# Kernel optimization log

Measured on AMD Instinct MI355X. Metric: run time of the kernel, lower is better.

The kernel has to match this reference:

```python
import jax, jax.numpy as jnp
import numpy as np

B, K, S, E = 16, 16, 512, 512   # batch, k_history, max_spikes_in_batch, embed_dim
L, H, KVH, D = 16, 8, 2, 64     # num_latents, heads, kv heads, head_dim
BIN = 50                        # bin_size (RoPE table length)


def setup_inputs() -> dict:
    key = jax.random.key(0)
    ks = jax.random.split(key, 8)
    spike = jax.random.normal(ks[0], (B, K, S, E), dtype=jnp.float32)
    offsets = jax.random.randint(ks[1], (B, K, S), 0, BIN)
    spike_lengths = jax.random.randint(ks[2], (B, K), 1, S + 1)  # >=1 so no fully-masked row
    # standard RoPE tables of shape (BIN, D)
    inv_freq = 1.0 / (10000.0 ** (np.arange(0, D, 2, dtype=np.float32) / D))
    freqs = np.outer(np.arange(BIN, dtype=np.float32), inv_freq)      # (BIN, D/2)
    emb = np.concatenate([freqs, freqs], axis=-1)                     # (BIN, D)
    cos = jnp.asarray(np.cos(emb), dtype=jnp.float32)
    sin = jnp.asarray(np.sin(emb), dtype=jnp.float32)
    latent_query = jax.random.normal(ks[3], (L, E), dtype=jnp.float32)
    Wq = jax.random.normal(ks[4], (H * D, E), dtype=jnp.float32) * (E ** -0.5)
    Wk = jax.random.normal(ks[5], (KVH * D, E), dtype=jnp.float32) * (E ** -0.5)
    Wv = jax.random.normal(ks[6], (KVH * D, E), dtype=jnp.float32) * (E ** -0.5)
    Wo = jax.random.normal(ks[7], (E, H * D), dtype=jnp.float32) * ((H * D) ** -0.5)
    return dict(spike=spike, offsets=offsets, spike_lengths=spike_lengths,
                cos=cos, sin=sin, latent_query=latent_query,
                Wq=Wq, Wk=Wk, Wv=Wv, Wo=Wo)


def rotate_half(x):
    h = x.shape[-1] // 2
    return jnp.concatenate([-x[..., h:], x[..., :h]], axis=-1)


def reference(spike, offsets, spike_lengths, cos, sin, latent_query, Wq, Wk, Wv, Wo):
    n_rep = H // KVH
    # fixed learnable queries, shared across batch / k_history
    xq = (latent_query @ Wq.T).reshape(L, H, D)                         # (L,H,D)
    xk = jnp.einsum('bkse,he->bksh', spike, Wk).reshape(B, K, S, KVH, D)
    xv = jnp.einsum('bkse,he->bksh', spike, Wv).reshape(B, K, S, KVH, D)
    # inline RoPE on keys only (is_decoder=False), driven by per-token offsets
    cos_sel = cos[offsets][..., None, :]                                # (B,K,S,1,D)
    sin_sel = sin[offsets][..., None, :]
    xk = xk * cos_sel + rotate_half(xk) * sin_sel
    # repeat_kv: interleaved head repetition (matches torch expand+reshape)
    xk = jnp.repeat(xk, n_rep, axis=3)                                  # (B,K,S,H,D)
    xv = jnp.repeat(xv, n_rep, axis=3)
    scores = jnp.einsum('lhd,bkshd->bkhls', xq, xk) / jnp.sqrt(jnp.float32(D))
    # ragged-length mask: positions >= spike_lengths are invalid
    pos = jnp.arange(S)
    mask = pos[None, None, None, None, :] >= spike_lengths[:, :, None, None, None]
    scores = jnp.where(mask, -jnp.inf, scores)
    attn = jax.nn.softmax(scores, axis=-1)                              # (B,K,H,L,S)
    out = jnp.einsum('bkhls,bkshd->bklhd', attn, xv).reshape(B, K, L, H * D)
    return out @ Wo.T                                                   # (B,K,L,E)
```

## Files before the change

### kernel.cpp

```cpp
#include <hip/hip_runtime.h>
#include <hip/hip_bf16.h>
#include <stdint.h>

typedef __attribute__((ext_vector_type(8))) short bf16x8;
typedef __attribute__((ext_vector_type(4))) float f32x4;

union FragU { uint4 u; bf16x8 v; };

#define Bn 16
#define Kn 16
#define Sn 512
#define En 512
#define Ln 16
#define Hn 8
#define Dn 64
#define BKTOT 256
#define MTOT (BKTOT*Sn)

__device__ __forceinline__ uint32_t pack_bf16(float lo, float hi) {
  uint32_t a = __float_as_uint(lo) + 0x8000u;
  uint32_t b = __float_as_uint(hi) + 0x8000u;
  return __builtin_amdgcn_perm(b, a, 0x07060302u);
}
__device__ __forceinline__ uint16_t bf16_1(float x) {
  __hip_bfloat16 h = __float2bfloat16(x);
  return *(uint16_t*)&h;
}
__device__ __forceinline__ void gload_lds16(const void* g, void* l) {
  __builtin_amdgcn_global_load_lds(
      (const __attribute__((address_space(1))) uint32_t*)g,
      (__attribute__((address_space(3))) uint32_t*)l, 16, 0, 0);
}

__global__ __launch_bounds__(256)
void xq_kernel(const float* __restrict__ latent, const float* __restrict__ Wq,
               float* __restrict__ xq)
{
  const int j = blockIdx.x;
  const int t = threadIdx.x;
  const float w0 = Wq[j*En + t];
  const float w1 = Wq[j*En + t + 256];
  float part[Ln];
#pragma unroll
  for (int l = 0; l < Ln; ++l)
    part[l] = w0 * latent[l*En + t] + w1 * latent[l*En + t + 256];
#pragma unroll
  for (int l = 0; l < Ln; ++l) {
    float v = part[l];
#pragma unroll
    for (int off = 32; off > 0; off >>= 1) v += __shfl_down(v, off, 64);
    part[l] = v;
  }
  __shared__ float red[4][Ln];
  const int lane = t & 63, wv = t >> 6;
  if (lane == 0) {
#pragma unroll
    for (int l = 0; l < Ln; ++l) red[wv][l] = part[l];
  }
  __syncthreads();
  if (t < Ln)
    xq[t*En + j] = red[0][t] + red[1][t] + red[2][t] + red[3][t];
}

__global__ __launch_bounds__(256)
void wconv_kernel(const float* __restrict__ Wk, const float* __restrict__ Wv,
                  const float* __restrict__ Wo,
                  uint4* __restrict__ Wsw, uint4* __restrict__ Wob)
{
  const int t = threadIdx.x;
  const int b = blockIdx.x;
  if (b < 64) {
    const int idx = b*256 + t;
    const int kb = idx >> 11;
    const int rem = idx & 2047;
    const int n = rem >> 3, p = rem & 7;
    const int c = p ^ (n & 7);
    const float* src = (n < 128 ? Wk + (size_t)n*En : Wv + (size_t)(n-128)*En) + kb*64 + c*8;
    float4 v0 = *(const float4*)src;
    float4 v1 = *(const float4*)(src+4);
    uint4 o;
    o.x = pack_bf16(v0.x,v0.y); o.y = pack_bf16(v0.z,v0.w);
    o.z = pack_bf16(v1.x,v1.y); o.w = pack_bf16(v1.z,v1.w);
    Wsw[idx] = o;
  } else {
    const int idx = (b-64)*256 + t;
    const float* src = Wo + (size_t)idx*8;
    float4 v0 = *(const float4*)src;
    float4 v1 = *(const float4*)(src+4);
    uint4 o;
    o.x = pack_bf16(v0.x,v0.y); o.y = pack_bf16(v0.z,v0.w);
    o.z = pack_bf16(v1.x,v1.y); o.w = pack_bf16(v1.z,v1.w);
    Wob[idx] = o;
  }
}

__global__ __launch_bounds__(256)
void kvproj_kernel(const float* __restrict__ spike, const int* __restrict__ offsets,
                   const float* __restrict__ cosT, const float* __restrict__ sinT,
                   const uint4* __restrict__ Wsw, const int* __restrict__ lengths,
                   uint16_t* __restrict__ Kbuf, uint16_t* __restrict__ Vt)
{
  __shared__ __align__(16) uint16_t Bs[256*64];
  __shared__ __align__(16) uint16_t As[64*72];
  const int t = threadIdx.x;
  const int bk   = blockIdx.x >> 3;
  const int tile = blockIdx.x & 7;
  if (tile * 64 >= lengths[bk]) return;
  const int m0 = blockIdx.x * 64;
  const int lane = t & 63, wv = t >> 6;
  const int quad = lane >> 4, lr = lane & 15;

  f32x4 acc[4][4];
#pragma unroll
  for (int i=0;i<4;i++)
#pragma unroll
    for (int j=0;j<4;j++) acc[i][j] = (f32x4){0.f,0.f,0.f,0.f};

  const int arow = t >> 3;
  const int aseg = t & 7;

  for (int kb = 0; kb < 8; ++kb) {
    const char* gb = (const char*)(Wsw + kb*2048) + (wv*64 + lane)*16;
    char* lb = (char*)Bs + wv*1024;
#pragma unroll
    for (int i = 0; i < 8; ++i)
      gload_lds16(gb + i*4096, lb + i*4096);
#pragma unroll
    for (int j = 0; j < 2; ++j) {
      const int row = arow + 32*j;
      const float* src = &spike[(size_t)(m0+row)*En + kb*64 + aseg*8];
      float4 v0 = *(const float4*)src;
      float4 v1 = *(const float4*)(src+4);
      uint4 o;
      o.x = pack_bf16(v0.x,v0.y); o.y = pack_bf16(v0.z,v0.w);
      o.z = pack_bf16(v1.x,v1.y); o.w = pack_bf16(v1.z,v1.w);
      *(uint4*)&As[row*72 + aseg*8] = o;
    }
    __syncthreads();
#pragma unroll
    for (int kk = 0; kk < 2; ++kk) {
      const int c = kk*4 + quad;
      FragU aF[4], bF[4];
#pragma unroll
      for (int mi=0;mi<4;mi++) aF[mi].u = *(const uint4*)&As[(mi*16+lr)*72 + c*8];
#pragma unroll
      for (int ni=0;ni<4;ni++) {
        const int n = wv*64 + ni*16 + lr;
        bF[ni].u = *(const uint4*)&Bs[n*64 + (c ^ (n&7))*8];
      }
#pragma unroll
      for (int mi=0;mi<4;mi++)
#pragma unroll
        for (int ni=0;ni<4;ni++)
          acc[mi][ni] = __builtin_amdgcn_mfma_f32_16x16x32_bf16(aF[mi].v, bF[ni].v, acc[mi][ni], 0,0,0);
    }
    __syncthreads();
  }

  const int sbase = m0 & 511;
  if (wv < 2) {
#pragma unroll
    for (int mi=0;mi<4;mi++) {
#pragma unroll
      for (int r=0;r<4;r++) {
        const int s = sbase + mi*16 + quad*4 + r;
        const int off = offsets[m0 + mi*16 + quad*4 + r];
#pragma unroll
        for (int ni=0;ni<4;ni++) {
          const int d = ni*16 + lr;
          const float v = acc[mi][ni][r];
          const float p = acc[mi][ni^2][r];
          const float rot = (ni < 2) ? -p : p;
          const float cc  = cosT[off*Dn + d];
          const float sn  = sinT[off*Dn + d];
          Kbuf[((size_t)(bk*512 + s))*128 + wv*64 + d] = bf16_1(v*cc + rot*sn);
        }
      }
    }
  } else {
    const int nbase = (wv - 2) * 64;
#pragma unroll
    for (int mi=0;mi<4;mi++) {
#pragma unroll
      for (int ni=0;ni<4;ni++) {
        const int np = nbase + ni*16 + lr;
        const int s  = sbase + mi*16 + quad*4;
        uint2 pk;
        pk.x = pack_bf16(acc[mi][ni][0], acc[mi][ni][1]);
        pk.y = pack_bf16(acc[mi][ni][2], acc[mi][ni][3]);
        *(uint2*)&Vt[((size_t)(bk*128 + np))*512 + s] = pk;
      }
    }
  }
}

__global__ __launch_bounds__(256)
void attn_kernel(const float* __restrict__ xq, const uint16_t* __restrict__ Kbuf,
                 const uint16_t* __restrict__ Vt, const int* __restrict__ lengths,
                 uint16_t* __restrict__ attn_out)
{
  __shared__ __align__(16) uint16_t Ks [128*72];
  __shared__ __align__(16) uint16_t Vts[64*136];
  __shared__ __align__(16) uint16_t Ps [4*16*136];

  const int t = threadIdx.x;
  const int bk = blockIdx.x >> 1, kvh = blockIdx.x & 1;
  const int w = t >> 6, lane = t & 63;
  const int quad = lane >> 4, lr = lane & 15;
  const int h = kvh*4 + w;
  const int len = lengths[bk];

  FragU aQ[2];
#pragma unroll
  for (int kk=0;kk<2;kk++) {
    const float* qp = &xq[lr*En + h*Dn + kk*32 + quad*8];
    float4 q0 = *(const float4*)qp;
    float4 q1 = *(const float4*)(qp + 4);
    aQ[kk].u.x = pack_bf16(q0.x*0.125f, q0.y*0.125f);
    aQ[kk].u.y = pack_bf16(q0.z*0.125f, q0.w*0.125f);
    aQ[kk].u.z = pack_bf16(q1.x*0.125f, q1.y*0.125f);
    aQ[kk].u.w = pack_bf16(q1.z*0.125f, q1.w*0.125f);
  }

  float m_run[4], l_run[4], alpha[4];
  f32x4 oacc[4];
#pragma unroll
  for (int r=0;r<4;r++){ m_run[r] = -3.0e38f; l_run[r] = 0.f; }
#pragma unroll
  for (int nd=0;nd<4;nd++) oacc[nd] = (f32x4){0.f,0.f,0.f,0.f};

  const int krow = t >> 1, kseg = t & 1;
  const int vrow = t >> 2, vseg = t & 3;

  for (int c = 0; c < 4; ++c) {
    const int s0 = c * 128;
    if (s0 >= len) break;
    __syncthreads();
    {
      const uint16_t* g = &Kbuf[((size_t)(bk*512 + s0 + krow))*128 + kvh*64 + kseg*32];
      uint16_t* dst = &Ks[krow*72 + kseg*32];
      uint4 a0 = *(const uint4*)g, a1 = *(const uint4*)(g+8);
      uint4 a2 = *(const uint4*)(g+16), a3 = *(const uint4*)(g+24);
      *(uint4*)dst = a0; *(uint4*)(dst+8) = a1; *(uint4*)(dst+16) = a2; *(uint4*)(dst+24) = a3;

      const uint16_t* gv = &Vt[((size_t)(bk*128 + kvh*64 + vrow))*512 + s0 + vseg*32];
      uint16_t* dv = &Vts[vrow*136 + vseg*32];
      uint4 b0 = *(const uint4*)gv, b1 = *(const uint4*)(gv+8);
      uint4 b2 = *(const uint4*)(gv+16), b3 = *(const uint4*)(gv+24);
      *(uint4*)dv = b0; *(uint4*)(dv+8) = b1; *(uint4*)(dv+16) = b2; *(uint4*)(dv+24) = b3;
    }
    __syncthreads();

    f32x4 sc[8];
#pragma unroll
    for (int ni=0;ni<8;ni++) {
      FragU b0, b1;
      b0.u = *(const uint4*)&Ks[(ni*16+lr)*72 + quad*8];
      b1.u = *(const uint4*)&Ks[(ni*16+lr)*72 + 32 + quad*8];
      f32x4 a = (f32x4){0.f,0.f,0.f,0.f};
      a = __builtin_amdgcn_mfma_f32_16x16x32_bf16(aQ[0].v, b0.v, a, 0,0,0);
      a = __builtin_amdgcn_mfma_f32_16x16x32_bf16(aQ[1].v, b1.v, a, 0,0,0);
      sc[ni] = a;
    }
#pragma unroll
    for (int ni=0;ni<8;ni++)
      if (s0 + ni*16 + lr >= len)
        sc[ni] = (f32x4){-3.0e38f,-3.0e38f,-3.0e38f,-3.0e38f};

#pragma unroll
    for (int r=0;r<4;r++) {
      float mx = sc[0][r];
#pragma unroll
      for (int ni=1;ni<8;ni++) mx = fmaxf(mx, sc[ni][r]);
#pragma unroll
      for (int o=1;o<16;o<<=1) mx = fmaxf(mx, __shfl_xor(mx, o, 16));
      const float mnew = fmaxf(m_run[r], mx);
      alpha[r] = __expf(m_run[r] - mnew);
      m_run[r] = mnew;
      float ssum = 0.f;
#pragma unroll
      for (int ni=0;ni<8;ni++) {
        float p = __expf(sc[ni][r] - mnew);
        sc[ni][r] = p;
        ssum += p;
      }
#pragma unroll
      for (int o=1;o<16;o<<=1) ssum += __shfl_xor(ssum, o, 16);
      l_run[r] = l_run[r]*alpha[r] + ssum;
    }

#pragma unroll
    for (int ni=0;ni<8;ni++)
#pragma unroll
      for (int r=0;r<4;r++)
        Ps[(w*16 + quad*4 + r)*136 + ni*16 + lr] = bf16_1(sc[ni][r]);

#pragma unroll
    for (int nd=0;nd<4;nd++)
#pragma unroll
      for (int r=0;r<4;r++) oacc[nd][r] *= alpha[r];

#pragma unroll
    for (int kk=0;kk<4;kk++) {
      FragU aP;
      aP.u = *(const uint4*)&Ps[(w*16 + lr)*136 + kk*32 + quad*8];
#pragma unroll
      for (int nd=0;nd<4;nd++) {
        FragU bV;
        bV.u = *(const uint4*)&Vts[(nd*16+lr)*136 + kk*32 + quad*8];
        oacc[nd] = __builtin_amdgcn_mfma_f32_16x16x32_bf16(aP.v, bV.v, oacc[nd], 0,0,0);
      }
    }
  }

#pragma unroll
  for (int r=0;r<4;r++) {
    const float rs = 1.0f / l_run[r];
    const int l = quad*4 + r;
#pragma unroll
    for (int nd=0;nd<4;nd++)
      attn_out[((size_t)(bk*16 + l))*512 + h*64 + nd*16 + lr] = bf16_1(oacc[nd][r] * rs);
  }
}

__global__ __launch_bounds__(256)
void oproj_kernel(const uint16_t* __restrict__ Ab, const uint16_t* __restrict__ Wob,
                  float* __restrict__ out)
{
  __shared__ __align__(16) uint16_t As[128*72];
  __shared__ __align__(16) uint16_t Bs[128*72];
  const int t = threadIdx.x;
  const int m0 = (blockIdx.x >> 2) * 128;
  const int n0 = (blockIdx.x & 3) * 128;
  const int lane = t & 63, wv = t >> 6;
  const int quad = lane >> 4, lr = lane & 15;
  const int wm = wv >> 1, wn = wv & 1;

  f32x4 acc[4][4];
#pragma unroll
  for (int i=0;i<4;i++)
#pragma unroll
    for (int j=0;j<4;j++) acc[i][j] = (f32x4){0.f,0.f,0.f,0.f};

  const int srow = t >> 3, sseg = t & 7;
  for (int kb = 0; kb < 8; ++kb) {
#pragma unroll
    for (int j = 0; j < 4; ++j) {
      const int row = srow + 32*j;
      *(uint4*)&As[row*72 + sseg*8] = *(const uint4*)&Ab [(size_t)(m0+row)*512 + kb*64 + sseg*8];
      *(uint4*)&Bs[row*72 + sseg*8] = *(const uint4*)&Wob[(size_t)(n0+row)*512 + kb*64 + sseg*8];
    }
    __syncthreads();
#pragma unroll
    for (int kk = 0; kk < 2; ++kk) {
      const int c = kk*4 + quad;
      FragU aF[4], bF[4];
#pragma unroll
      for (int mi=0;mi<4;mi++) aF[mi].u = *(const uint4*)&As[(wm*64+mi*16+lr)*72 + c*8];
#pragma unroll
      for (int ni=0;ni<4;ni++) bF[ni].u = *(const uint4*)&Bs[(wn*64+ni*16+lr)*72 + c*8];
#pragma unroll
      for (int mi=0;mi<4;mi++)
#pragma unroll
        for (int ni=0;ni<4;ni++)
          acc[mi][ni] = __builtin_amdgcn_mfma_f32_16x16x32_bf16(aF[mi].v, bF[ni].v, acc[mi][ni], 0,0,0);
    }
    __syncthreads();
  }
#pragma unroll
  for (int mi=0;mi<4;mi++)
#pragma unroll
    for (int r=0;r<4;r++)
#pragma unroll
      for (int ni=0;ni<4;ni++)
        out[(size_t)(m0 + wm*64 + mi*16 + quad*4 + r)*512 + n0 + wn*64 + ni*16 + lr] = acc[mi][ni][r];
}

extern "C" void kernel_launch(void* const* d_in, const int* in_sizes, int n_in,
                              void* d_out, int out_size, void* d_ws, size_t ws_size,
                              hipStream_t stream)
{
  const float* spike   = (const float*)d_in[0];
  const int*   offsets = (const int*)d_in[1];
  const int*   lengths = (const int*)d_in[2];
  const float* cosT    = (const float*)d_in[3];
  const float* sinT    = (const float*)d_in[4];
  const float* latent  = (const float*)d_in[5];
  const float* Wq      = (const float*)d_in[6];
  const float* Wk      = (const float*)d_in[7];
  const float* Wv      = (const float*)d_in[8];
  const float* Wo      = (const float*)d_in[9];
  float* out = (float*)d_out;

  char* ws = (char*)d_ws;
  float*    xq   = (float*)ws;
  uint4*    Wsw  = (uint4*)(ws + 65536);
  uint4*    Wob  = (uint4*)(ws + 65536 + 262144);
  uint16_t* Kbuf = (uint16_t*)(ws + 1048576);
  uint16_t* Vt   = (uint16_t*)(ws + 1048576 + 33554432ull);
  uint16_t* attn_out = (uint16_t*)(ws + 1048576 + 67108864ull);

  hipLaunchKernelGGL(xq_kernel,     dim3(512),  dim3(256), 0, stream, latent, Wq, xq);
  hipLaunchKernelGGL(wconv_kernel,  dim3(192),  dim3(256), 0, stream, Wk, Wv, Wo, Wsw, Wob);
  hipLaunchKernelGGL(kvproj_kernel, dim3(2048), dim3(256), 0, stream, spike, offsets, cosT, sinT, Wsw, lengths, Kbuf, Vt);
  hipLaunchKernelGGL(attn_kernel,   dim3(512),  dim3(256), 0, stream, xq, Kbuf, Vt, lengths, attn_out);
  hipLaunchKernelGGL(oproj_kernel,  dim3(128),  dim3(256), 0, stream, attn_out, (const uint16_t*)Wob, out);
}
```

Before: 431.7 us.

## Prefetch next tiles into registers across kvproj, attention and output projection; merge prep kernels

```diff
diff --git a/kernel.cpp b/kernel.cpp
--- a/kernel.cpp
+++ b/kernel.cpp
@@ -14,8 +14,6 @@
 #define Ln 16
 #define Hn 8
 #define Dn 64
-#define BKTOT 256
-#define MTOT (BKTOT*Sn)
 
 __device__ __forceinline__ uint32_t pack_bf16(float lo, float hi) {
   uint32_t a = __float_as_uint(lo) + 0x8000u;
@@ -33,44 +31,39 @@
 }
 
 __global__ __launch_bounds__(256)
-void xq_kernel(const float* __restrict__ latent, const float* __restrict__ Wq,
-               float* __restrict__ xq)
+void prep_kernel(const float* __restrict__ latent, const float* __restrict__ Wq,
+                 const float* __restrict__ Wk, const float* __restrict__ Wv,
+                 const float* __restrict__ Wo,
+                 float* __restrict__ xq, uint4* __restrict__ Wsw, uint4* __restrict__ Wob)
 {
-  const int j = blockIdx.x;
+  __shared__ float red[4][Ln];
   const int t = threadIdx.x;
-  const float w0 = Wq[j*En + t];
-  const float w1 = Wq[j*En + t + 256];
-  float part[Ln];
-#pragma unroll
-  for (int l = 0; l < Ln; ++l)
-    part[l] = w0 * latent[l*En + t] + w1 * latent[l*En + t + 256];
-#pragma unroll
-  for (int l = 0; l < Ln; ++l) {
-    float v = part[l];
-#pragma unroll
-    for (int off = 32; off > 0; off >>= 1) v += __shfl_down(v, off, 64);
-    part[l] = v;
-  }
-  __shared__ float red[4][Ln];
-  const int lane = t & 63, wv = t >> 6;
-  if (lane == 0) {
-#pragma unroll
-    for (int l = 0; l < Ln; ++l) red[wv][l] = part[l];
-  }
-  __syncthreads();
-  if (t < Ln)
-    xq[t*En + j] = red[0][t] + red[1][t] + red[2][t] + red[3][t];
-}
-
-__global__ __launch_bounds__(256)
-void wconv_kernel(const float* __restrict__ Wk, const float* __restrict__ Wv,
-                  const float* __restrict__ Wo,
-                  uint4* __restrict__ Wsw, uint4* __restrict__ Wob)
-{
-  const int t = threadIdx.x;
-  const int b = blockIdx.x;
-  if (b < 64) {
-    const int idx = b*256 + t;
+  const int blk = blockIdx.x;
+  if (blk < 512) {
+    const int j = blk;
+    const float w0 = Wq[j*En + t];
+    const float w1 = Wq[j*En + t + 256];
+    float part[Ln];
+#pragma unroll
+    for (int l = 0; l < Ln; ++l)
+      part[l] = w0 * latent[l*En + t] + w1 * latent[l*En + t + 256];
+#pragma unroll
+    for (int l = 0; l < Ln; ++l) {
+      float v = part[l];
+#pragma unroll
+      for (int off = 32; off > 0; off >>= 1) v += __shfl_down(v, off, 64);
+      part[l] = v;
+    }
+    const int lane = t & 63, wv = t >> 6;
+    if (lane == 0) {
+#pragma unroll
+      for (int l = 0; l < Ln; ++l) red[wv][l] = part[l];
+    }
+    __syncthreads();
+    if (t < Ln)
+      xq[t*En + j] = red[0][t] + red[1][t] + red[2][t] + red[3][t];
+  } else if (blk < 576) {
+    const int idx = (blk - 512)*256 + t;
     const int kb = idx >> 11;
     const int rem = idx & 2047;
     const int n = rem >> 3, p = rem & 7;
@@ -83,7 +76,7 @@
     o.z = pack_bf16(v1.x,v1.y); o.w = pack_bf16(v1.z,v1.w);
     Wsw[idx] = o;
   } else {
-    const int idx = (b-64)*256 + t;
+    const int idx = (blk - 576)*256 + t;
     const float* src = Wo + (size_t)idx*8;
     float4 v0 = *(const float4*)src;
     float4 v1 = *(const float4*)(src+4);
@@ -94,7 +87,7 @@
   }
 }
 
-__global__ __launch_bounds__(256)
+__global__ __launch_bounds__(256, 3)
 void kvproj_kernel(const float* __restrict__ spike, const int* __restrict__ offsets,
                    const float* __restrict__ cosT, const float* __restrict__ sinT,
                    const uint4* __restrict__ Wsw, const int* __restrict__ lengths,
@@ -119,24 +112,45 @@
   const int arow = t >> 3;
   const int aseg = t & 7;
 
+  float4 pf[4];
+  {
+    const float* s0p = &spike[(size_t)(m0+arow)*En + aseg*8];
+    pf[0] = *(const float4*)s0p; pf[1] = *(const float4*)(s0p+4);
+    const float* s1p = &spike[(size_t)(m0+arow+32)*En + aseg*8];
+    pf[2] = *(const float4*)s1p; pf[3] = *(const float4*)(s1p+4);
+  }
+
   for (int kb = 0; kb < 8; ++kb) {
     const char* gb = (const char*)(Wsw + kb*2048) + (wv*64 + lane)*16;
     char* lb = (char*)Bs + wv*1024;
 #pragma unroll
     for (int i = 0; i < 8; ++i)
       gload_lds16(gb + i*4096, lb + i*4096);
-#pragma unroll
-    for (int j = 0; j < 2; ++j) {
-      const int row = arow + 32*j;
-      const float* src = &spike[(size_t)(m0+row)*En + kb*64 + aseg*8];
-      float4 v0 = *(const float4*)src;
-      float4 v1 = *(const float4*)(src+4);
+
+    {
       uint4 o;
-      o.x = pack_bf16(v0.x,v0.y); o.y = pack_bf16(v0.z,v0.w);
-      o.z = pack_bf16(v1.x,v1.y); o.w = pack_bf16(v1.z,v1.w);
-      *(uint4*)&As[row*72 + aseg*8] = o;
-    }
-    __syncthreads();
+      o.x = pack_bf16(pf[0].x,pf[0].y); o.y = pack_bf16(pf[0].z,pf[0].w);
+      o.z = pack_bf16(pf[1].x,pf[1].y); o.w = pack_bf16(pf[1].z,pf[1].w);
+      *(uint4*)&As[arow*72 + aseg*8] = o;
+      uint4 p;
+      p.x = pack_bf16(pf[2].x,pf[2].y); p.y = pack_bf16(pf[2].z,pf[2].w);
+      p.z = pack_bf16(pf[3].x,pf[3].y); p.w = pack_bf16(pf[3].z,pf[3].w);
+      *(uint4*)&As[(arow+32)*72 + aseg*8] = p;
+    }
+
+    __builtin_amdgcn_sched_barrier(0);
+    if (kb < 7) {
+      const float* s0p = &spike[(size_t)(m0+arow)*En + (kb+1)*64 + aseg*8];
+      pf[0] = *(const float4*)s0p; pf[1] = *(const float4*)(s0p+4);
+      const float* s1p = &spike[(size_t)(m0+arow+32)*En + (kb+1)*64 + aseg*8];
+      pf[2] = *(const float4*)s1p; pf[3] = *(const float4*)(s1p+4);
+      asm volatile("s_waitcnt vmcnt(4) lgkmcnt(0)" ::: "memory");
+    } else {
+      asm volatile("s_waitcnt vmcnt(0) lgkmcnt(0)" ::: "memory");
+    }
+    __builtin_amdgcn_s_barrier();
+    __builtin_amdgcn_sched_barrier(0);
+
 #pragma unroll
     for (int kk = 0; kk < 2; ++kk) {
       const int c = kk*4 + quad;
@@ -154,7 +168,10 @@
         for (int ni=0;ni<4;ni++)
           acc[mi][ni] = __builtin_amdgcn_mfma_f32_16x16x32_bf16(aF[mi].v, bF[ni].v, acc[mi][ni], 0,0,0);
     }
-    __syncthreads();
+
+    asm volatile("s_waitcnt lgkmcnt(0)" ::: "memory");
+    __builtin_amdgcn_s_barrier();
+    __builtin_amdgcn_sched_barrier(0);
   }
 
   const int sbase = m0 & 511;
@@ -209,6 +226,7 @@
   const int quad = lane >> 4, lr = lane & 15;
   const int h = kvh*4 + w;
   const int len = lengths[bk];
+  const int nc = (len + 127) >> 7;
 
   FragU aQ[2];
 #pragma unroll
@@ -231,27 +249,30 @@
 
   const int krow = t >> 1, kseg = t & 1;
   const int vrow = t >> 2, vseg = t & 3;
-
-  for (int c = 0; c < 4; ++c) {
+  const uint16_t* gK = &Kbuf[((size_t)(bk*512 + krow))*128 + kvh*64 + kseg*32];
+  const uint16_t* gV = &Vt [((size_t)(bk*128 + kvh*64 + vrow))*512 + vseg*32];
+
+  auto pref = [&](int c, uint4* r) {
+    const uint16_t* g  = gK + (size_t)c*16384;
+    r[0] = *(const uint4*)g;      r[1] = *(const uint4*)(g+8);
+    r[2] = *(const uint4*)(g+16); r[3] = *(const uint4*)(g+24);
+    const uint16_t* gv = gV + c*128;
+    r[4] = *(const uint4*)gv;      r[5] = *(const uint4*)(gv+8);
+    r[6] = *(const uint4*)(gv+16); r[7] = *(const uint4*)(gv+24);
+  };
+  auto stage = [&](const uint4* r) {
+    uint16_t* dst = &Ks[krow*72 + kseg*32];
+    *(uint4*)dst = r[0]; *(uint4*)(dst+8) = r[1];
+    *(uint4*)(dst+16) = r[2]; *(uint4*)(dst+24) = r[3];
+    uint16_t* dv = &Vts[vrow*136 + vseg*32];
+    *(uint4*)dv = r[4]; *(uint4*)(dv+8) = r[5];
+    *(uint4*)(dv+16) = r[6]; *(uint4*)(dv+24) = r[7];
+  };
+
+  auto compute_chunk = [&](int c) {
     const int s0 = c * 128;
-    if (s0 >= len) break;
-    __syncthreads();
-    {
-      const uint16_t* g = &Kbuf[((size_t)(bk*512 + s0 + krow))*128 + kvh*64 + kseg*32];
-      uint16_t* dst = &Ks[krow*72 + kseg*32];
-      uint4 a0 = *(const uint4*)g, a1 = *(const uint4*)(g+8);
-      uint4 a2 = *(const uint4*)(g+16), a3 = *(const uint4*)(g+24);
-      *(uint4*)dst = a0; *(uint4*)(dst+8) = a1; *(uint4*)(dst+16) = a2; *(uint4*)(dst+24) = a3;
-
-      const uint16_t* gv = &Vt[((size_t)(bk*128 + kvh*64 + vrow))*512 + s0 + vseg*32];
-      uint16_t* dv = &Vts[vrow*136 + vseg*32];
-      uint4 b0 = *(const uint4*)gv, b1 = *(const uint4*)(gv+8);
-      uint4 b2 = *(const uint4*)(gv+16), b3 = *(const uint4*)(gv+24);
-      *(uint4*)dv = b0; *(uint4*)(dv+8) = b1; *(uint4*)(dv+16) = b2; *(uint4*)(dv+24) = b3;
-    }
-    __syncthreads();
-
     f32x4 sc[8];
+    __builtin_amdgcn_s_setprio(1);
 #pragma unroll
     for (int ni=0;ni<8;ni++) {
       FragU b0, b1;
@@ -262,6 +283,7 @@
       a = __builtin_amdgcn_mfma_f32_16x16x32_bf16(aQ[1].v, b1.v, a, 0,0,0);
       sc[ni] = a;
     }
+    __builtin_amdgcn_s_setprio(0);
 #pragma unroll
     for (int ni=0;ni<8;ni++)
       if (s0 + ni*16 + lr >= len)
@@ -300,6 +322,7 @@
 #pragma unroll
       for (int r=0;r<4;r++) oacc[nd][r] *= alpha[r];
 
+    __builtin_amdgcn_s_setprio(1);
 #pragma unroll
     for (int kk=0;kk<4;kk++) {
       FragU aP;
@@ -311,7 +334,25 @@
         oacc[nd] = __builtin_amdgcn_mfma_f32_16x16x32_bf16(aP.v, bV.v, oacc[nd], 0,0,0);
       }
     }
-  }
+    __builtin_amdgcn_s_setprio(0);
+  };
+
+  auto run_chunk = [&](int c, uint4* cur, uint4* nxt) {
+    __syncthreads();
+    stage(cur);
+    if (c + 1 < nc) pref(c + 1, nxt);
+    asm volatile("s_waitcnt lgkmcnt(0)" ::: "memory");
+    __builtin_amdgcn_s_barrier();
+    __builtin_amdgcn_sched_barrier(0);
+    compute_chunk(c);
+  };
+
+  uint4 bufA[8], bufB[8];
+  pref(0, bufA);
+  run_chunk(0, bufA, bufB);
+  if (nc > 1) run_chunk(1, bufB, bufA);
+  if (nc > 2) run_chunk(2, bufA, bufB);
+  if (nc > 3) run_chunk(3, bufB, bufA);
 
 #pragma unroll
   for (int r=0;r<4;r++) {
@@ -327,53 +368,75 @@
 void oproj_kernel(const uint16_t* __restrict__ Ab, const uint16_t* __restrict__ Wob,
                   float* __restrict__ out)
 {
-  __shared__ __align__(16) uint16_t As[128*72];
-  __shared__ __align__(16) uint16_t Bs[128*72];
+  __shared__ __align__(16) uint16_t As[64*72];
+  __shared__ __align__(16) uint16_t Bs[64*72];
   const int t = threadIdx.x;
-  const int m0 = (blockIdx.x >> 2) * 128;
-  const int n0 = (blockIdx.x & 3) * 128;
+  const int m0 = (blockIdx.x >> 3) * 64;
+  const int n0 = (blockIdx.x & 7) * 64;
   const int lane = t & 63, wv = t >> 6;
   const int quad = lane >> 4, lr = lane & 15;
   const int wm = wv >> 1, wn = wv & 1;
 
-  f32x4 acc[4][4];
-#pragma unroll
-  for (int i=0;i<4;i++)
-#pragma unroll
-    for (int j=0;j<4;j++) acc[i][j] = (f32x4){0.f,0.f,0.f,0.f};
+  f32x4 acc[2][2];
+#pragma unroll
+  for (int i=0;i<2;i++)
+#pragma unroll
+    for (int j=0;j<2;j++) acc[i][j] = (f32x4){0.f,0.f,0.f,0.f};
 
   const int srow = t >> 3, sseg = t & 7;
+
+  uint4 pa[2], pb[2];
+#pragma unroll
+  for (int j = 0; j < 2; ++j) {
+    const int row = srow + 32*j;
+    pa[j] = *(const uint4*)&Ab [(size_t)(m0+row)*512 + sseg*8];
+    pb[j] = *(const uint4*)&Wob[(size_t)(n0+row)*512 + sseg*8];
+  }
+
   for (int kb = 0; kb < 8; ++kb) {
 #pragma unroll
-    for (int j = 0; j < 4; ++j) {
+    for (int j = 0; j < 2; ++j) {
       const int row = srow + 32*j;
-      *(uint4*)&As[row*72 + sseg*8] = *(const uint4*)&Ab [(size_t)(m0+row)*512 + kb*64 + sseg*8];
-      *(uint4*)&Bs[row*72 + sseg*8] = *(const uint4*)&Wob[(size_t)(n0+row)*512 + kb*64 + sseg*8];
-    }
-    __syncthreads();
+      *(uint4*)&As[row*72 + sseg*8] = pa[j];
+      *(uint4*)&Bs[row*72 + sseg*8] = pb[j];
+    }
+    __builtin_amdgcn_sched_barrier(0);
+    if (kb < 7) {
+#pragma unroll
+      for (int j = 0; j < 2; ++j) {
+        const int row = srow + 32*j;
+        pa[j] = *(const uint4*)&Ab [(size_t)(m0+row)*512 + (kb+1)*64 + sseg*8];
+        pb[j] = *(const uint4*)&Wob[(size_t)(n0+row)*512 + (kb+1)*64 + sseg*8];
+      }
+    }
+    asm volatile("s_waitcnt lgkmcnt(0)" ::: "memory");
+    __builtin_amdgcn_s_barrier();
+    __builtin_amdgcn_sched_barrier(0);
 #pragma unroll
     for (int kk = 0; kk < 2; ++kk) {
       const int c = kk*4 + quad;
-      FragU aF[4], bF[4];
-#pragma unroll
-      for (int mi=0;mi<4;mi++) aF[mi].u = *(const uint4*)&As[(wm*64+mi*16+lr)*72 + c*8];
-#pragma unroll
-      for (int ni=0;ni<4;ni++) bF[ni].u = *(const uint4*)&Bs[(wn*64+ni*16+lr)*72 + c*8];
-#pragma unroll
-      for (int mi=0;mi<4;mi++)
-#pragma unroll
-        for (int ni=0;ni<4;ni++)
+      FragU aF[2], bF[2];
+#pragma unroll
+      for (int mi=0;mi<2;mi++) aF[mi].u = *(const uint4*)&As[(wm*32+mi*16+lr)*72 + c*8];
+#pragma unroll
+      for (int ni=0;ni<2;ni++) bF[ni].u = *(const uint4*)&Bs[(wn*32+ni*16+lr)*72 + c*8];
+#pragma unroll
+      for (int mi=0;mi<2;mi++)
+#pragma unroll
+        for (int ni=0;ni<2;ni++)
           acc[mi][ni] = __builtin_amdgcn_mfma_f32_16x16x32_bf16(aF[mi].v, bF[ni].v, acc[mi][ni], 0,0,0);
     }
-    __syncthreads();
-  }
-#pragma unroll
-  for (int mi=0;mi<4;mi++)
+    asm volatile("s_waitcnt lgkmcnt(0)" ::: "memory");
+    __builtin_amdgcn_s_barrier();
+    __builtin_amdgcn_sched_barrier(0);
+  }
+#pragma unroll
+  for (int mi=0;mi<2;mi++)
 #pragma unroll
     for (int r=0;r<4;r++)
 #pragma unroll
-      for (int ni=0;ni<4;ni++)
-        out[(size_t)(m0 + wm*64 + mi*16 + quad*4 + r)*512 + n0 + wn*64 + ni*16 + lr] = acc[mi][ni][r];
+      for (int ni=0;ni<2;ni++)
+        out[(size_t)(m0 + wm*32 + mi*16 + quad*4 + r)*512 + n0 + wn*32 + ni*16 + lr] = acc[mi][ni][r];
 }
 
 extern "C" void kernel_launch(void* const* d_in, const int* in_sizes, int n_in,
@@ -400,9 +463,12 @@
   uint16_t* Vt   = (uint16_t*)(ws + 1048576 + 33554432ull);
   uint16_t* attn_out = (uint16_t*)(ws + 1048576 + 67108864ull);
 
-  hipLaunchKernelGGL(xq_kernel,     dim3(512),  dim3(256), 0, stream, latent, Wq, xq);
-  hipLaunchKernelGGL(wconv_kernel,  dim3(192),  dim3(256), 0, stream, Wk, Wv, Wo, Wsw, Wob);
-  hipLaunchKernelGGL(kvproj_kernel, dim3(2048), dim3(256), 0, stream, spike, offsets, cosT, sinT, Wsw, lengths, Kbuf, Vt);
-  hipLaunchKernelGGL(attn_kernel,   dim3(512),  dim3(256), 0, stream, xq, Kbuf, Vt, lengths, attn_out);
-  hipLaunchKernelGGL(oproj_kernel,  dim3(128),  dim3(256), 0, stream, attn_out, (const uint16_t*)Wob, out);
-}
+  hipLaunchKernelGGL(prep_kernel,   dim3(704),  dim3(256), 0, stream,
+                     latent, Wq, Wk, Wv, Wo, xq, Wsw, Wob);
+  hipLaunchKernelGGL(kvproj_kernel, dim3(2048), dim3(256), 0, stream,
+                     spike, offsets, cosT, sinT, Wsw, lengths, Kbuf, Vt);
+  hipLaunchKernelGGL(attn_kernel,   dim3(512),  dim3(256), 0, stream,
+                     xq, Kbuf, Vt, lengths, attn_out);
+  hipLaunchKernelGGL(oproj_kernel,  dim3(512),  dim3(256), 0, stream,
+                     attn_out, (const uint16_t*)Wob, out);
+}
```

Measured after the change: 441.8 us. 1.02x slower.

## Merge prep kernels and register-prefetch next K/V chunk in attention

Applied to the files above, without the earlier changes.

```diff
diff --git a/kernel.cpp b/kernel.cpp
--- a/kernel.cpp
+++ b/kernel.cpp
@@ -14,8 +14,6 @@
 #define Ln 16
 #define Hn 8
 #define Dn 64
-#define BKTOT 256
-#define MTOT (BKTOT*Sn)
 
 __device__ __forceinline__ uint32_t pack_bf16(float lo, float hi) {
   uint32_t a = __float_as_uint(lo) + 0x8000u;
@@ -33,44 +31,39 @@
 }
 
 __global__ __launch_bounds__(256)
-void xq_kernel(const float* __restrict__ latent, const float* __restrict__ Wq,
-               float* __restrict__ xq)
+void prep_kernel(const float* __restrict__ latent, const float* __restrict__ Wq,
+                 const float* __restrict__ Wk, const float* __restrict__ Wv,
+                 const float* __restrict__ Wo,
+                 float* __restrict__ xq, uint4* __restrict__ Wsw, uint4* __restrict__ Wob)
 {
-  const int j = blockIdx.x;
+  __shared__ float red[4][Ln];
   const int t = threadIdx.x;
-  const float w0 = Wq[j*En + t];
-  const float w1 = Wq[j*En + t + 256];
-  float part[Ln];
-#pragma unroll
-  for (int l = 0; l < Ln; ++l)
-    part[l] = w0 * latent[l*En + t] + w1 * latent[l*En + t + 256];
-#pragma unroll
-  for (int l = 0; l < Ln; ++l) {
-    float v = part[l];
-#pragma unroll
-    for (int off = 32; off > 0; off >>= 1) v += __shfl_down(v, off, 64);
-    part[l] = v;
-  }
-  __shared__ float red[4][Ln];
-  const int lane = t & 63, wv = t >> 6;
-  if (lane == 0) {
-#pragma unroll
-    for (int l = 0; l < Ln; ++l) red[wv][l] = part[l];
-  }
-  __syncthreads();
-  if (t < Ln)
-    xq[t*En + j] = red[0][t] + red[1][t] + red[2][t] + red[3][t];
-}
-
-__global__ __launch_bounds__(256)
-void wconv_kernel(const float* __restrict__ Wk, const float* __restrict__ Wv,
-                  const float* __restrict__ Wo,
-                  uint4* __restrict__ Wsw, uint4* __restrict__ Wob)
-{
-  const int t = threadIdx.x;
-  const int b = blockIdx.x;
-  if (b < 64) {
-    const int idx = b*256 + t;
+  const int blk = blockIdx.x;
+  if (blk < 512) {
+    const int j = blk;
+    const float w0 = Wq[j*En + t];
+    const float w1 = Wq[j*En + t + 256];
+    float part[Ln];
+#pragma unroll
+    for (int l = 0; l < Ln; ++l)
+      part[l] = w0 * latent[l*En + t] + w1 * latent[l*En + t + 256];
+#pragma unroll
+    for (int l = 0; l < Ln; ++l) {
+      float v = part[l];
+#pragma unroll
+      for (int off = 32; off > 0; off >>= 1) v += __shfl_down(v, off, 64);
+      part[l] = v;
+    }
+    const int lane = t & 63, wv = t >> 6;
+    if (lane == 0) {
+#pragma unroll
+      for (int l = 0; l < Ln; ++l) red[wv][l] = part[l];
+    }
+    __syncthreads();
+    if (t < Ln)
+      xq[t*En + j] = red[0][t] + red[1][t] + red[2][t] + red[3][t];
+  } else if (blk < 576) {
+    const int idx = (blk - 512)*256 + t;
     const int kb = idx >> 11;
     const int rem = idx & 2047;
     const int n = rem >> 3, p = rem & 7;
@@ -83,7 +76,7 @@
     o.z = pack_bf16(v1.x,v1.y); o.w = pack_bf16(v1.z,v1.w);
     Wsw[idx] = o;
   } else {
-    const int idx = (b-64)*256 + t;
+    const int idx = (blk - 576)*256 + t;
     const float* src = Wo + (size_t)idx*8;
     float4 v0 = *(const float4*)src;
     float4 v1 = *(const float4*)(src+4);
@@ -209,6 +202,7 @@
   const int quad = lane >> 4, lr = lane & 15;
   const int h = kvh*4 + w;
   const int len = lengths[bk];
+  const int nc = (len + 127) >> 7;
 
   FragU aQ[2];
 #pragma unroll
@@ -231,27 +225,41 @@
 
   const int krow = t >> 1, kseg = t & 1;
   const int vrow = t >> 2, vseg = t & 3;
-
-  for (int c = 0; c < 4; ++c) {
+  const uint16_t* gK = &Kbuf[((size_t)(bk*512 + krow))*128 + kvh*64 + kseg*32];
+  const uint16_t* gV = &Vt [((size_t)(bk*128 + kvh*64 + vrow))*512 + vseg*32];
+
+  uint4 k0, k1, k2, k3, v0, v1, v2, v3;
+
+#define PREF(c) do {                                           \
+    const uint16_t* g_  = gK + (size_t)(c)*16384;              \
+    k0 = *(const uint4*)g_;      k1 = *(const uint4*)(g_+8);   \
+    k2 = *(const uint4*)(g_+16); k3 = *(const uint4*)(g_+24);  \
+    const uint16_t* gv_ = gV + (c)*128;                        \
+    v0 = *(const uint4*)gv_;      v1 = *(const uint4*)(gv_+8); \
+    v2 = *(const uint4*)(gv_+16); v3 = *(const uint4*)(gv_+24);\
+  } while(0)
+
+  PREF(0);
+
+  for (int c = 0; c < nc; ++c) {
     const int s0 = c * 128;
-    if (s0 >= len) break;
     __syncthreads();
     {
-      const uint16_t* g = &Kbuf[((size_t)(bk*512 + s0 + krow))*128 + kvh*64 + kseg*32];
       uint16_t* dst = &Ks[krow*72 + kseg*32];
-      uint4 a0 = *(const uint4*)g, a1 = *(const uint4*)(g+8);
-      uint4 a2 = *(const uint4*)(g+16), a3 = *(const uint4*)(g+24);
-      *(uint4*)dst = a0; *(uint4*)(dst+8) = a1; *(uint4*)(dst+16) = a2; *(uint4*)(dst+24) = a3;
-
-      const uint16_t* gv = &Vt[((size_t)(bk*128 + kvh*64 + vrow))*512 + s0 + vseg*32];
+      *(uint4*)dst = k0; *(uint4*)(dst+8) = k1;
+      *(uint4*)(dst+16) = k2; *(uint4*)(dst+24) = k3;
       uint16_t* dv = &Vts[vrow*136 + vseg*32];
-      uint4 b0 = *(const uint4*)gv, b1 = *(const uint4*)(gv+8);
-      uint4 b2 = *(const uint4*)(gv+16), b3 = *(const uint4*)(gv+24);
-      *(uint4*)dv = b0; *(uint4*)(dv+8) = b1; *(uint4*)(dv+16) = b2; *(uint4*)(dv+24) = b3;
-    }
-    __syncthreads();
+      *(uint4*)dv = v0; *(uint4*)(dv+8) = v1;
+      *(uint4*)(dv+16) = v2; *(uint4*)(dv+24) = v3;
+    }
+    if (c + 1 < nc) PREF(c + 1);
+    __builtin_amdgcn_sched_barrier(0);
+    asm volatile("s_waitcnt lgkmcnt(0)" ::: "memory");
+    __builtin_amdgcn_s_barrier();
+    __builtin_amdgcn_sched_barrier(0);
 
     f32x4 sc[8];
+    __builtin_amdgcn_s_setprio(1);
 #pragma unroll
     for (int ni=0;ni<8;ni++) {
       FragU b0, b1;
@@ -262,6 +270,7 @@
       a = __builtin_amdgcn_mfma_f32_16x16x32_bf16(aQ[1].v, b1.v, a, 0,0,0);
       sc[ni] = a;
     }
+    __builtin_amdgcn_s_setprio(0);
 #pragma unroll
     for (int ni=0;ni<8;ni++)
       if (s0 + ni*16 + lr >= len)
@@ -300,6 +309,7 @@
 #pragma unroll
       for (int r=0;r<4;r++) oacc[nd][r] *= alpha[r];
 
+    __builtin_amdgcn_s_setprio(1);
 #pragma unroll
     for (int kk=0;kk<4;kk++) {
       FragU aP;
@@ -311,7 +321,9 @@
         oacc[nd] = __builtin_amdgcn_mfma_f32_16x16x32_bf16(aP.v, bV.v, oacc[nd], 0,0,0);
       }
     }
-  }
+    __builtin_amdgcn_s_setprio(0);
+  }
+#undef PREF
 
 #pragma unroll
   for (int r=0;r<4;r++) {
@@ -400,9 +412,12 @@
   uint16_t* Vt   = (uint16_t*)(ws + 1048576 + 33554432ull);
   uint16_t* attn_out = (uint16_t*)(ws + 1048576 + 67108864ull);
 
-  hipLaunchKernelGGL(xq_kernel,     dim3(512),  dim3(256), 0, stream, latent, Wq, xq);
-  hipLaunchKernelGGL(wconv_kernel,  dim3(192),  dim3(256), 0, stream, Wk, Wv, Wo, Wsw, Wob);
-  hipLaunchKernelGGL(kvproj_kernel, dim3(2048), dim3(256), 0, stream, spike, offsets, cosT, sinT, Wsw, lengths, Kbuf, Vt);
-  hipLaunchKernelGGL(attn_kernel,   dim3(512),  dim3(256), 0, stream, xq, Kbuf, Vt, lengths, attn_out);
-  hipLaunchKernelGGL(oproj_kernel,  dim3(128),  dim3(256), 0, stream, attn_out, (const uint16_t*)Wob, out);
-}
+  hipLaunchKernelGGL(prep_kernel,   dim3(704),  dim3(256), 0, stream,
+                     latent, Wq, Wk, Wv, Wo, xq, Wsw, Wob);
+  hipLaunchKernelGGL(kvproj_kernel, dim3(2048), dim3(256), 0, stream,
+                     spike, offsets, cosT, sinT, Wsw, lengths, Kbuf, Vt);
+  hipLaunchKernelGGL(attn_kernel,   dim3(512),  dim3(256), 0, stream,
+                     xq, Kbuf, Vt, lengths, attn_out);
+  hipLaunchKernelGGL(oproj_kernel,  dim3(128),  dim3(256), 0, stream,
+                     attn_out, (const uint16_t*)Wob, out);
+}
```

Measured after the change: 427.5 us. No clear change (-1.0%).
